# Kernel optimization log

Measured on AMD Instinct MI355X. Metric: run time of the kernel, lower is better.

The kernel has to match this reference:

```python
import jax, jax.numpy as jnp
import numpy as np

N = 65536      # total nodes (BS graphs of 4096 nodes)
E = 524288     # edges
BS = 16
EPS = 1e-5
D_ATT = 8      # attention d_model
H_ATT = 4      # attention heads
SQRT_D = np.float32(np.sqrt(8.0))


def gcn_conv(x, src, dst, W, b):
    # PyG GCNConv: add self-loops, sym-normalized sum aggregation of x @ W
    n = x.shape[0]
    h = x @ W  # [N, out]
    loop = jnp.arange(n, dtype=src.dtype)
    s = jnp.concatenate([src, loop])
    d = jnp.concatenate([dst, loop])
    deg = jax.ops.segment_sum(jnp.ones_like(d, x.dtype), d, num_segments=n)
    dinv = jax.lax.rsqrt(jnp.maximum(deg, 1.0))  # deg >= 1 due to self loops
    norm = dinv[s] * dinv[d]                      # [E+N]
    out = jax.ops.segment_sum(h[s] * norm[:, None], d, num_segments=n)
    return out + b


def sage_conv(x, src, dst, Wl, Wr, b):
    # PyG SAGEConv (mean aggr): lin_l(mean_{j in N(i)} x_j) + lin_r(x_i)
    n = x.shape[0]
    agg = jax.ops.segment_sum(x[src], dst, num_segments=n)
    cnt = jax.ops.segment_sum(jnp.ones_like(dst, x.dtype), dst, num_segments=n)
    mean = agg / jnp.maximum(cnt, 1.0)[:, None]
    return mean @ Wl + x @ Wr + b


def batch_norm(x):
    # F.batch_norm(x, None, None, training=True): per-feature, no affine, biased var
    mu = x.mean(axis=0)
    var = x.var(axis=0)
    return (x - mu) * jax.lax.rsqrt(var + EPS)


def attention_plug(plug, Wq, bq, Wk, bk, Wv, bv, Wfc, bfc):
    q = (plug @ Wq + bq).reshape(BS, 1, H_ATT, D_ATT)
    k = (plug @ Wk + bk).reshape(BS, 1, H_ATT, D_ATT)
    v = (plug @ Wv + bv).reshape(BS, 1, H_ATT, D_ATT)
    scores = jnp.einsum('bihd,bijd->bihj', q, k) / SQRT_D  # [BS,1,H,H]
    logits = scores[:, 0]                                   # squeeze -> [BS,H,H]
    u = jax.random.uniform(jax.random.key(42), logits.shape, minval=1e-9, maxval=1.0)
    gumbel = -jnp.log(-jnp.log(u))
    attn = jax.nn.softmax(logits + gumbel, axis=-1) * SQRT_D  # gumbel_softmax(tau=1)
    attn = attn.reshape(BS, 1, H_ATT, H_ATT)
    out = jnp.einsum('bihj,bijd->bihd', attn, v)  # [BS,1,H,D]
    out = out.reshape(BS, D_ATT, H_ATT).reshape(BS, D_ATT * H_ATT)  # view then flatten
    return out @ Wfc + bfc  # [BS, 4]


def setup_inputs():
    key = jax.random.key(0)
    ks = jax.random.split(key, 24)
    w = lambda k, shp, fan: (jax.random.normal(k, shp, jnp.float32) / np.sqrt(fan)).astype(jnp.float32)
    inp = {}
    inp['x'] = jax.random.normal(ks[0], (N, 640), jnp.float32)
    inp['edge_index'] = jax.random.randint(ks[1], (2, E), 0, N, jnp.int32)
    inp['gender'] = jax.random.uniform(ks[2], (BS, 2), jnp.float32)
    inp['age'] = jax.random.uniform(ks[3], (BS, 1), jnp.float32)
    inp['handed'] = jax.random.uniform(ks[4], (BS, 5), jnp.float32)
    inp['W1'] = w(ks[5], (640, 320), 640); inp['b1'] = jnp.zeros((320,), jnp.float32)
    inp['Wl2'] = w(ks[6], (320, 180), 320); inp['Wr2'] = w(ks[7], (320, 180), 320); inp['b2'] = jnp.zeros((180,), jnp.float32)
    inp['Wl3'] = w(ks[8], (180, 90), 180); inp['Wr3'] = w(ks[9], (180, 90), 180); inp['b3'] = jnp.zeros((90,), jnp.float32)
    inp['Wl4'] = w(ks[10], (90, 50), 90); inp['Wr4'] = w(ks[11], (90, 50), 90); inp['b4'] = jnp.zeros((50,), jnp.float32)
    inp['Wq'] = w(ks[12], (8, 32), 8); inp['bq'] = jnp.zeros((32,), jnp.float32)
    inp['Wk'] = w(ks[13], (8, 32), 8); inp['bk'] = jnp.zeros((32,), jnp.float32)
    inp['Wv'] = w(ks[14], (8, 32), 8); inp['bv'] = jnp.zeros((32,), jnp.float32)
    inp['Wfc'] = w(ks[15], (32, 4), 32); inp['bfc'] = jnp.zeros((4,), jnp.float32)
    inp['Wf1'] = w(ks[16], (54, 32), 54); inp['bf1'] = jnp.zeros((32,), jnp.float32)
    inp['Wf2'] = w(ks[17], (32, 16), 32); inp['bf2'] = jnp.zeros((16,), jnp.float32)
    inp['Wf3'] = w(ks[18], (16, 1), 16); inp['bf3'] = jnp.zeros((1,), jnp.float32)
    return inp


def reference(x, edge_index, gender, age, handed,
              W1, b1, Wl2, Wr2, b2, Wl3, Wr3, b3, Wl4, Wr4, b4,
              Wq, bq, Wk, bk, Wv, bv, Wfc, bfc,
              Wf1, bf1, Wf2, bf2, Wf3, bf3):
    src, dst = edge_index[0], edge_index[1]
    h = batch_norm(jax.nn.leaky_relu(gcn_conv(x, src, dst, W1, b1)))
    h = batch_norm(jax.nn.leaky_relu(sage_conv(h, src, dst, Wl2, Wr2, b2)))
    h = batch_norm(jax.nn.leaky_relu(sage_conv(h, src, dst, Wl3, Wr3, b3)))
    h = batch_norm(jax.nn.leaky_relu(sage_conv(h, src, dst, Wl4, Wr4, b4)))
    batch = jnp.arange(N) // (N // BS)
    pooled = jax.ops.segment_sum(h, batch, num_segments=BS)  # global_add_pool [BS,50]
    plug = jnp.concatenate([gender, age, handed], axis=1)    # [BS,8]
    plugx = attention_plug(plug, Wq, bq, Wk, bk, Wv, bv, Wfc, bfc)  # [BS,4]
    emb = jnp.concatenate([pooled, plugx], axis=1)           # [BS,54]
    out = ((emb @ Wf1 + bf1) @ Wf2 + bf2) @ Wf3 + bf3        # [BS,1]
    return out, emb
```

## Files before the change

### kernel.cpp

```cpp
#include <hip/hip_runtime.h>
#include <cstdint>

#define NN 65536
#define EE 524288
#define BS_ 16

typedef unsigned short u16;
typedef unsigned int u32;
typedef __attribute__((ext_vector_type(8))) short short8v;
typedef __attribute__((ext_vector_type(4))) float f32x4;

__device__ __forceinline__ u16 f2bf(float f) {
    u32 u = __float_as_uint(f);
    u32 r = (u + 0x7fffu + ((u >> 16) & 1u)) >> 16;
    return (u16)r;
}
__device__ __forceinline__ float bff(u16 h) {
    return __uint_as_float(((u32)h) << 16);
}

__device__ __forceinline__ float bnleaky(float v, float s, float q) {
    const float invN = 1.0f / 65536.0f;
    float mu = s * invN;
    float var = q * invN - mu * mu;
    float u = v >= 0.f ? v : 0.01f * v;
    return (u - mu) * rsqrtf(var + 1e-5f);
}

__device__ __forceinline__ u32 rotl32(u32 x, int d) {
    return (x << d) | (x >> (32 - d));
}
__device__ __forceinline__ void threefry_0_42(u32& x0, u32& x1) {
    const u32 ks0 = 0u, ks1 = 42u, ks2 = 0u ^ 42u ^ 0x1BD11BDAu;
    x0 += ks0; x1 += ks1;
#define RND(r) { x0 += x1; x1 = rotl32(x1, r); x1 ^= x0; }
    RND(13) RND(15) RND(26) RND(6)  x0 += ks1; x1 += ks2 + 1u;
    RND(17) RND(29) RND(16) RND(24) x0 += ks2; x1 += ks0 + 2u;
    RND(13) RND(15) RND(26) RND(6)  x0 += ks0; x1 += ks1 + 3u;
    RND(17) RND(29) RND(16) RND(24) x0 += ks1; x1 += ks2 + 4u;
    RND(13) RND(15) RND(26) RND(6)  x0 += ks2; x1 += ks0 + 5u;
#undef RND
}

__global__ void k_indeg(const int* __restrict__ dst, int* __restrict__ indeg) {
    int e = blockIdx.x * 256 + threadIdx.x;
    if (e < EE) atomicAdd(&indeg[dst[e]], 1);
}

__global__ void k_scan(const int* __restrict__ indeg, int* __restrict__ rowptr,
                       int* __restrict__ cursor) {
    __shared__ int psum[256];
    int t = threadIdx.x;
    int base = t * 256;
    int s = 0;
    for (int i = 0; i < 256; ++i) s += indeg[base + i];
    psum[t] = s;
    __syncthreads();
    for (int off = 1; off < 256; off <<= 1) {
        int v = (t >= off) ? psum[t - off] : 0;
        __syncthreads();
        psum[t] += v;
        __syncthreads();
    }
    int run = (t == 0) ? 0 : psum[t - 1];
    for (int i = 0; i < 256; ++i) {
        rowptr[base + i] = run;
        cursor[base + i] = run;
        run += indeg[base + i];
    }
    if (t == 255) rowptr[NN] = run;
}

__global__ void k_fill(const int* __restrict__ src, const int* __restrict__ dst,
                       int* __restrict__ cursor, int* __restrict__ csr) {
    int e = blockIdx.x * 256 + threadIdx.x;
    if (e < EE) {
        int d = dst[e];
        int p = atomicAdd(&cursor[d], 1);
        csr[p] = src[e];
    }
}

__global__ void k_dinv(const int* __restrict__ indeg, float* __restrict__ dinv) {
    int i = blockIdx.x * 256 + threadIdx.x;
    if (i < NN) dinv[i] = rsqrtf((float)indeg[i] + 1.0f);
}

__global__ void k_wsplit2(const float* __restrict__ Wr, const float* __restrict__ Wlsrc,
                          int K, int N, int KP, int CS, int NPW,
                          u16* __restrict__ Wh, u16* __restrict__ Wl) {
    int idx = blockIdx.x * 256 + threadIdx.x;
    if (idx >= NPW * KP) return;
    int n = idx / KP, k = idx % KP;
    float v = 0.f;
    if (n < CS) {
        if (n < N && k < K) v = Wr[(size_t)k * N + n];
    } else {
        int n2 = n - CS;
        if (Wlsrc != nullptr && n2 < N && k < K) v = Wlsrc[(size_t)k * N + n2];
    }
    u16 h = f2bf(v);
    u16 l = f2bf(v - bff(h));
    Wh[idx] = h;
    Wl[idx] = l;
}

template <bool HASB, bool HASBN>
__global__ __launch_bounds__(256, 2) void k_gemm_mfma(
    const float* __restrict__ A, const u16* __restrict__ Wgh, const u16* __restrict__ Wgl,
    int KP, int lda, const float* __restrict__ bns,
    const float* __restrict__ bias, float* __restrict__ O1, float* __restrict__ O2,
    int N, int CS) {
    __shared__ u16 Ah[64][72];
    __shared__ u16 Al[64][72];
    __shared__ u16 Wh[128][72];
    __shared__ u16 Wl[128][72];

    const int t = threadIdx.x;
    const int bm = blockIdx.x * 64;
    const int bn = blockIdx.y * 128;
    const int lane = t & 63;
    const int wid = t >> 6;
    const int wr = wid >> 1, wc = wid & 1;

    f32x4 acc[2][4];
#pragma unroll
    for (int m = 0; m < 2; ++m)
#pragma unroll
        for (int n = 0; n < 4; ++n) acc[m][n] = (f32x4){0.f, 0.f, 0.f, 0.f};

    const int sr = t >> 4;
    const int sc4 = (t & 15) * 4;

    for (int k0 = 0; k0 < KP; k0 += 64) {
        float4 s4, q4;
        if (HASBN) {
            s4 = *(const float4*)(bns + k0 + sc4);
            q4 = *(const float4*)(bns + 512 + k0 + sc4);
        }
#pragma unroll
        for (int p = 0; p < 4; ++p) {
            int rr = sr + 16 * p;
            const float4 v = *(const float4*)(A + (size_t)(bm + rr) * lda + k0 + sc4);
            float vx = v.x, vy = v.y, vz = v.z, vw = v.w;
            if (HASBN) {
                vx = bnleaky(vx, s4.x, q4.x);
                vy = bnleaky(vy, s4.y, q4.y);
                vz = bnleaky(vz, s4.z, q4.z);
                vw = bnleaky(vw, s4.w, q4.w);
            }
            u16 h0 = f2bf(vx), h1 = f2bf(vy), h2 = f2bf(vz), h3 = f2bf(vw);
            u16 l0 = f2bf(vx - bff(h0)), l1 = f2bf(vy - bff(h1));
            u16 l2 = f2bf(vz - bff(h2)), l3 = f2bf(vw - bff(h3));
            uint2 hh, ll;
            hh.x = (u32)h0 | ((u32)h1 << 16); hh.y = (u32)h2 | ((u32)h3 << 16);
            ll.x = (u32)l0 | ((u32)l1 << 16); ll.y = (u32)l2 | ((u32)l3 << 16);
            *(uint2*)&Ah[rr][sc4] = hh;
            *(uint2*)&Al[rr][sc4] = ll;
        }
#pragma unroll
        for (int p = 0; p < 8; ++p) {
            int nn = sr + 16 * p;
            size_t go = (size_t)(bn + nn) * KP + k0 + sc4;
            *(uint2*)&Wh[nn][sc4] = *(const uint2*)(Wgh + go);
            *(uint2*)&Wl[nn][sc4] = *(const uint2*)(Wgl + go);
        }
        __syncthreads();
        const int fr = lane & 15;
        const int kg = (lane >> 4) * 8;
#pragma unroll
        for (int kk = 0; kk < 64; kk += 32) {
            short8v a_h[2], a_l[2], w_h[4], w_l[4];
#pragma unroll
            for (int m = 0; m < 2; ++m) {
                a_h[m] = *(const short8v*)&Ah[wr * 32 + m * 16 + fr][kk + kg];
                a_l[m] = *(const short8v*)&Al[wr * 32 + m * 16 + fr][kk + kg];
            }
#pragma unroll
            for (int n = 0; n < 4; ++n) {
                w_h[n] = *(const short8v*)&Wh[wc * 64 + n * 16 + fr][kk + kg];
                w_l[n] = *(const short8v*)&Wl[wc * 64 + n * 16 + fr][kk + kg];
            }
#pragma unroll
            for (int m = 0; m < 2; ++m)
#pragma unroll
                for (int n = 0; n < 4; ++n) {
                    acc[m][n] = __builtin_amdgcn_mfma_f32_16x16x32_bf16(a_h[m], w_h[n], acc[m][n], 0, 0, 0);
                    acc[m][n] = __builtin_amdgcn_mfma_f32_16x16x32_bf16(a_h[m], w_l[n], acc[m][n], 0, 0, 0);
                    acc[m][n] = __builtin_amdgcn_mfma_f32_16x16x32_bf16(a_l[m], w_h[n], acc[m][n], 0, 0, 0);
                }
        }
        __syncthreads();
    }
    const int fr = lane & 15, fq = lane >> 4;
#pragma unroll
    for (int m = 0; m < 2; ++m) {
        int row = bm + wr * 32 + m * 16 + fq * 4;
#pragma unroll
        for (int n = 0; n < 4; ++n) {
            int col = bn + wc * 64 + n * 16 + fr;
            if (col < CS) {
                float b = (HASB && col < N) ? bias[col] : 0.f;
#pragma unroll
                for (int e = 0; e < 4; ++e)
                    O1[(size_t)(row + e) * CS + col] = acc[m][n][e] + b;
            } else if (O2 != nullptr) {
                int c2 = col - CS;
#pragma unroll
                for (int e = 0; e < 4; ++e)
                    O2[(size_t)(row + e) * CS + c2] = acc[m][n][e];
            }
        }
    }
}

__global__ __launch_bounds__(256) void k_gcn_agg320(const float* __restrict__ h,
                                                    const int* __restrict__ rowptr,
                                                    const int* __restrict__ csr,
                                                    const float* __restrict__ dinv,
                                                    const float* __restrict__ bias,
                                                    float* __restrict__ out) {
    int lane = threadIdx.x & 63;
    int n = blockIdx.x * 4 + (threadIdx.x >> 6);
    bool has1 = lane < 16;
    float di = dinv[n];
    float s2 = di * di;
    const float4* hn = (const float4*)(h + (size_t)n * 320);
    float4 v0 = hn[lane];
    float4 a0 = make_float4(v0.x * s2, v0.y * s2, v0.z * s2, v0.w * s2);
    float4 a1 = make_float4(0.f, 0.f, 0.f, 0.f);
    if (has1) {
        float4 v1 = hn[64 + lane];
        a1 = make_float4(v1.x * s2, v1.y * s2, v1.z * s2, v1.w * s2);
    }
    int e = rowptr[n], e1 = rowptr[n + 1];
    for (; e + 4 <= e1; e += 4) {
        int s0 = csr[e], s1 = csr[e + 1], s2i = csr[e + 2], s3 = csr[e + 3];
        float w0 = dinv[s0] * di, w1 = dinv[s1] * di, w2 = dinv[s2i] * di, w3 = dinv[s3] * di;
        const float4* p0 = (const float4*)(h + (size_t)s0 * 320);
        const float4* p1 = (const float4*)(h + (size_t)s1 * 320);
        const float4* p2 = (const float4*)(h + (size_t)s2i * 320);
        const float4* p3 = (const float4*)(h + (size_t)s3 * 320);
        float4 u0 = p0[lane], u1 = p1[lane], u2 = p2[lane], u3 = p3[lane];
        a0.x += u0.x * w0 + u1.x * w1 + u2.x * w2 + u3.x * w3;
        a0.y += u0.y * w0 + u1.y * w1 + u2.y * w2 + u3.y * w3;
        a0.z += u0.z * w0 + u1.z * w1 + u2.z * w2 + u3.z * w3;
        a0.w += u0.w * w0 + u1.w * w1 + u2.w * w2 + u3.w * w3;
        if (has1) {
            float4 x0 = p0[64 + lane], x1 = p1[64 + lane], x2 = p2[64 + lane], x3 = p3[64 + lane];
            a1.x += x0.x * w0 + x1.x * w1 + x2.x * w2 + x3.x * w3;
            a1.y += x0.y * w0 + x1.y * w1 + x2.y * w2 + x3.y * w3;
            a1.z += x0.z * w0 + x1.z * w1 + x2.z * w2 + x3.z * w3;
            a1.w += x0.w * w0 + x1.w * w1 + x2.w * w2 + x3.w * w3;
        }
    }
    for (; e < e1; ++e) {
        int s = csr[e];
        float w = dinv[s] * di;
        const float4* hs = (const float4*)(h + (size_t)s * 320);
        float4 u0 = hs[lane];
        a0.x = fmaf(u0.x, w, a0.x); a0.y = fmaf(u0.y, w, a0.y);
        a0.z = fmaf(u0.z, w, a0.z); a0.w = fmaf(u0.w, w, a0.w);
        if (has1) {
            float4 u1 = hs[64 + lane];
            a1.x = fmaf(u1.x, w, a1.x); a1.y = fmaf(u1.y, w, a1.y);
            a1.z = fmaf(u1.z, w, a1.z); a1.w = fmaf(u1.w, w, a1.w);
        }
    }
    const float4* b4 = (const float4*)bias;
    float4* on = (float4*)(out + (size_t)n * 320);
    float4 bb = b4[lane];
    on[lane] = make_float4(a0.x + bb.x, a0.y + bb.y, a0.z + bb.z, a0.w + bb.w);
    if (has1) {
        float4 bb1 = b4[64 + lane];
        on[64 + lane] = make_float4(a1.x + bb1.x, a1.y + bb1.y, a1.z + bb1.z, a1.w + bb1.w);
    }
}

template <int CH, int LOG_NPW>
__global__ __launch_bounds__(256) void k_agg_add(const float* __restrict__ T,
                                                 const int* __restrict__ rowptr,
                                                 const int* __restrict__ csr,
                                                 const int* __restrict__ indeg,
                                                 float* __restrict__ C) {
    constexpr int NPW = 1 << LOG_NPW;
    constexpr int LPN = 64 >> LOG_NPW;
    constexpr int SC = CH * 4;
    int lane = threadIdx.x & 63;
    int sub = lane / LPN;
    int ch = lane & (LPN - 1);
    int n = (blockIdx.x * 4 + (threadIdx.x >> 6)) * NPW + sub;
    bool act = ch < CH;
    float4 acc = make_float4(0.f, 0.f, 0.f, 0.f);
    int e = rowptr[n], e1 = rowptr[n + 1];
    for (; e + 4 <= e1; e += 4) {
        int s0 = csr[e], s1 = csr[e + 1], s2 = csr[e + 2], s3 = csr[e + 3];
        if (act) {
            float4 u0 = *(const float4*)(T + (size_t)s0 * SC + ch * 4);
            float4 u1 = *(const float4*)(T + (size_t)s1 * SC + ch * 4);
            float4 u2 = *(const float4*)(T + (size_t)s2 * SC + ch * 4);
            float4 u3 = *(const float4*)(T + (size_t)s3 * SC + ch * 4);
            acc.x += (u0.x + u1.x) + (u2.x + u3.x);
            acc.y += (u0.y + u1.y) + (u2.y + u3.y);
            acc.z += (u0.z + u1.z) + (u2.z + u3.z);
            acc.w += (u0.w + u1.w) + (u2.w + u3.w);
        }
    }
    for (; e < e1; ++e) {
        int s = csr[e];
        if (act) {
            float4 u = *(const float4*)(T + (size_t)s * SC + ch * 4);
            acc.x += u.x; acc.y += u.y; acc.z += u.z; acc.w += u.w;
        }
    }
    int cnt = indeg[n];
    float inv = 1.0f / (float)(cnt > 1 ? cnt : 1);
    if (act) {
        float4* cp = (float4*)(C + (size_t)n * SC + ch * 4);
        float4 c = *cp;
        c.x = fmaf(acc.x, inv, c.x);
        c.y = fmaf(acc.y, inv, c.y);
        c.z = fmaf(acc.z, inv, c.z);
        c.w = fmaf(acc.w, inv, c.w);
        *cp = c;
    }
}

template <int D, int STR>
__global__ __launch_bounds__(256) void k_bn_stats(const float* __restrict__ x,
                                                  float* __restrict__ stats) {
    constexpr int NC = (D + 255) / 256;
    int t = threadIdx.x;
    int r0 = blockIdx.x * 64;
    float s[NC], q[NC];
#pragma unroll
    for (int i = 0; i < NC; ++i) { s[i] = 0.f; q[i] = 0.f; }
#pragma unroll 4
    for (int r = r0; r < r0 + 64; ++r) {
        const float* row = x + (size_t)r * STR;
#pragma unroll
        for (int i = 0; i < NC; ++i) {
            int c = t + 256 * i;
            if (c < D) {
                float v = row[c];
                v = v >= 0.f ? v : 0.01f * v;
                s[i] += v;
                q[i] += v * v;
            }
        }
    }
#pragma unroll
    for (int i = 0; i < NC; ++i) {
        int c = t + 256 * i;
        if (c < D) {
            atomicAdd(&stats[c], s[i]);
            atomicAdd(&stats[512 + c], q[i]);
        }
    }
}

template <int STR>
__global__ __launch_bounds__(256) void k_bn_apply(float* __restrict__ x,
                                                  const float* __restrict__ stats) {
    const float invN = 1.0f / (float)NN;
    size_t total4 = (size_t)NN * STR / 4;
    size_t stride = (size_t)gridDim.x * 256;
    for (size_t i = (size_t)blockIdx.x * 256 + threadIdx.x; i < total4; i += stride) {
        int c = (int)((i * 4) % STR);
        float4 v = ((const float4*)x)[i];
        float4 m4 = *(const float4*)(stats + c);
        float4 q4 = *(const float4*)(stats + 512 + c);
        float4 o;
        o.x = bnleaky(v.x, m4.x, q4.x);
        o.y = bnleaky(v.y, m4.y, q4.y);
        o.z = bnleaky(v.z, m4.z, q4.z);
        o.w = bnleaky(v.w, m4.w, q4.w);
        ((float4*)x)[i] = o;
    }
}

__global__ __launch_bounds__(256) void k_pool(const float* __restrict__ h,
                                              float* __restrict__ pooled) {
    int blk = blockIdx.x;
    int batch = blk >> 4, seg = blk & 15;
    int f = threadIdx.x & 63, g = threadIdx.x >> 6;
    size_t base = ((size_t)batch * 4096 + seg * 256 + g) * 64 + f;
    float acc = 0.f;
    for (int i = 0; i < 64; ++i) acc += h[base + (size_t)i * 256];
    atomicAdd(&pooled[batch * 64 + f], acc);
}

__global__ __launch_bounds__(256) void k_head(
    const float* __restrict__ gender, const float* __restrict__ age,
    const float* __restrict__ handed, const float* __restrict__ Wq,
    const float* __restrict__ bq, const float* __restrict__ Wk,
    const float* __restrict__ bk, const float* __restrict__ Wv,
    const float* __restrict__ bv, const float* __restrict__ Wfc,
    const float* __restrict__ bfc, const float* __restrict__ Wf1,
    const float* __restrict__ bf1, const float* __restrict__ Wf2,
    const float* __restrict__ bf2, const float* __restrict__ Wf3,
    const float* __restrict__ bf3, const float* __restrict__ pooled,
    float* __restrict__ dout) {
    __shared__ float plug[BS_][8];
    __shared__ float qs[BS_][32], ks[BS_][32], vs[BS_][32];
    __shared__ float gum[256];
    __shared__ float x32[BS_][32];
    __shared__ float px[BS_][4];
    __shared__ float embs[BS_][54];
    __shared__ float t1[BS_][32];
    __shared__ float t2[BS_][16];
    int t = threadIdx.x;

    if (t < 128) {
        int b = t >> 3, c = t & 7;
        float v;
        if (c < 2) v = gender[b * 2 + c];
        else if (c == 2) v = age[b];
        else v = handed[b * 5 + (c - 3)];
        plug[b][c] = v;
    }
    {
        u32 lane = (u32)(t & 127);
        u32 a = lane, b2 = lane + 128u;
        threefry_0_42(a, b2);
        u32 bits = (t < 128) ? a : b2;
        float u = __uint_as_float((bits >> 9) | 0x3f800000u) - 1.0f;
        const float mn = 1e-9f;
        u = u * (1.0f - mn) + mn;
        u = fmaxf(mn, u);
        gum[t] = -logf(-logf(u));
    }
    __syncthreads();
    for (int idx = t; idx < 512; idx += 256) {
        int b = idx >> 5, c = idx & 31;
        float aq = bq[c], ak = bk[c], av = bv[c];
#pragma unroll
        for (int i = 0; i < 8; ++i) {
            float p = plug[b][i];
            aq = fmaf(p, Wq[i * 32 + c], aq);
            ak = fmaf(p, Wk[i * 32 + c], ak);
            av = fmaf(p, Wv[i * 32 + c], av);
        }
        qs[b][c] = aq; ks[b][c] = ak; vs[b][c] = av;
    }
    __syncthreads();
    if (t < 64) {
        int b = t >> 2, h = t & 3;
        const float isq = 0.35355339059327373f;
        const float sq = 2.8284271247461903f;
        float sc[4];
#pragma unroll
        for (int j = 0; j < 4; ++j) {
            float d = 0.f;
#pragma unroll
            for (int dd = 0; dd < 8; ++dd) d = fmaf(qs[b][h * 8 + dd], ks[b][j * 8 + dd], d);
            sc[j] = d * isq + gum[b * 16 + h * 4 + j];
        }
        float m = fmaxf(fmaxf(sc[0], sc[1]), fmaxf(sc[2], sc[3]));
        float e0 = expf(sc[0] - m), e1 = expf(sc[1] - m), e2 = expf(sc[2] - m), e3 = expf(sc[3] - m);
        float sum = e0 + e1 + e2 + e3;
        float a0 = e0 / sum * sq, a1 = e1 / sum * sq, a2 = e2 / sum * sq, a3 = e3 / sum * sq;
#pragma unroll
        for (int dd = 0; dd < 8; ++dd) {
            float o = a0 * vs[b][0 * 8 + dd] + a1 * vs[b][1 * 8 + dd] +
                      a2 * vs[b][2 * 8 + dd] + a3 * vs[b][3 * 8 + dd];
            x32[b][h * 8 + dd] = o;
        }
    }
    __syncthreads();
    if (t < 64) {
        int b = t >> 2, n = t & 3;
        float a = bfc[n];
#pragma unroll
        for (int m = 0; m < 32; ++m) a = fmaf(x32[b][m], Wfc[m * 4 + n], a);
        px[b][n] = a;
    }
    __syncthreads();
    for (int idx = t; idx < BS_ * 54; idx += 256) {
        int b = idx / 54, c = idx % 54;
        float v = (c < 50) ? pooled[b * 64 + c] : px[b][c - 50];
        embs[b][c] = v;
        dout[16 + idx] = v;
    }
    __syncthreads();
    for (int idx = t; idx < 512; idx += 256) {
        int b = idx >> 5, c = idx & 31;
        float a = bf1[c];
#pragma unroll
        for (int k = 0; k < 54; ++k) a = fmaf(embs[b][k], Wf1[k * 32 + c], a);
        t1[b][c] = a;
    }
    __syncthreads();
    {
        int b = t >> 4, c = t & 15;
        float a = bf2[c];
#pragma unroll
        for (int k = 0; k < 32; ++k) a = fmaf(t1[b][k], Wf2[k * 16 + c], a);
        t2[b][c] = a;
    }
    __syncthreads();
    if (t < 16) {
        float a = bf3[0];
#pragma unroll
        for (int k = 0; k < 16; ++k) a = fmaf(t2[t][k], Wf3[k], a);
        dout[t] = a;
    }
}

extern "C" void kernel_launch(void* const* d_in, const int* in_sizes, int n_in,
                              void* d_out, int out_size, void* d_ws, size_t ws_size,
                              hipStream_t stream) {
    const float* x      = (const float*)d_in[0];
    const int*   ei     = (const int*)d_in[1];
    const float* gender = (const float*)d_in[2];
    const float* age    = (const float*)d_in[3];
    const float* handed = (const float*)d_in[4];
    const float* W1  = (const float*)d_in[5];
    const float* b1  = (const float*)d_in[6];
    const float* Wl2 = (const float*)d_in[7];
    const float* Wr2 = (const float*)d_in[8];
    const float* b2  = (const float*)d_in[9];
    const float* Wl3 = (const float*)d_in[10];
    const float* Wr3 = (const float*)d_in[11];
    const float* b3  = (const float*)d_in[12];
    const float* Wl4 = (const float*)d_in[13];
    const float* Wr4 = (const float*)d_in[14];
    const float* b4  = (const float*)d_in[15];
    const float* Wq  = (const float*)d_in[16];
    const float* bq  = (const float*)d_in[17];
    const float* Wk  = (const float*)d_in[18];
    const float* bk  = (const float*)d_in[19];
    const float* Wv  = (const float*)d_in[20];
    const float* bv  = (const float*)d_in[21];
    const float* Wfc = (const float*)d_in[22];
    const float* bfc = (const float*)d_in[23];
    const float* Wf1 = (const float*)d_in[24];
    const float* bf1 = (const float*)d_in[25];
    const float* Wf2 = (const float*)d_in[26];
    const float* bf2 = (const float*)d_in[27];
    const float* Wf3 = (const float*)d_in[28];
    const float* bf3 = (const float*)d_in[29];

    const int* srcp = ei;
    const int* dstp = ei + EE;

    char* wsb = (char*)d_ws;
    size_t off = 0;
    auto alloc = [&](size_t bytes) -> char* {
        char* p = wsb + off;
        off += (bytes + 255) & ~(size_t)255;
        return p;
    };
    float* P = (float*)alloc((size_t)NN * 320 * 4);
    float* Q = (float*)alloc((size_t)NN * 320 * 4);
    float* R = (float*)alloc((size_t)NN * 192 * 4);
    float* T = (float*)alloc((size_t)NN * 192 * 4);
    int* indeg  = (int*)alloc((size_t)NN * 4);
    int* rowptr = (int*)alloc((size_t)(NN + 1) * 4);
    int* cursor = (int*)alloc((size_t)(NN + 1) * 4);
    int* csr    = (int*)alloc((size_t)EE * 4);
    float* dinv = (float*)alloc((size_t)NN * 4);
    float* stats  = (float*)alloc(4096 * 4);
    float* pooled = (float*)alloc(16 * 64 * 4);
    u16* W1h = (u16*)alloc((size_t)384 * 640 * 2);
    u16* W1l = (u16*)alloc((size_t)384 * 640 * 2);
    u16* W2h = (u16*)alloc((size_t)384 * 320 * 2);
    u16* W2l = (u16*)alloc((size_t)384 * 320 * 2);
    u16* W3h = (u16*)alloc((size_t)256 * 192 * 2);
    u16* W3l = (u16*)alloc((size_t)256 * 192 * 2);
    u16* W4h = (u16*)alloc((size_t)128 * 128 * 2);
    u16* W4l = (u16*)alloc((size_t)128 * 128 * 2);
    float* dout = (float*)d_out;

    hipMemsetAsync(indeg, 0, (size_t)NN * 4, stream);
    hipMemsetAsync(stats, 0, 4096 * 4, stream);
    k_indeg<<<EE / 256, 256, 0, stream>>>(dstp, indeg);
    k_scan<<<1, 256, 0, stream>>>(indeg, rowptr, cursor);
    k_fill<<<EE / 256, 256, 0, stream>>>(srcp, dstp, cursor, csr);
    k_dinv<<<NN / 256, 256, 0, stream>>>(indeg, dinv);

    k_wsplit2<<<(384 * 640 + 255) / 256, 256, 0, stream>>>(W1, nullptr, 640, 320, 640, 320, 384, W1h, W1l);
    k_wsplit2<<<(384 * 320 + 255) / 256, 256, 0, stream>>>(Wr2, Wl2, 320, 180, 320, 192, 384, W2h, W2l);
    k_wsplit2<<<(256 * 192 + 255) / 256, 256, 0, stream>>>(Wr3, Wl3, 180, 90, 192, 128, 256, W3h, W3l);
    k_wsplit2<<<(128 * 128 + 255) / 256, 256, 0, stream>>>(Wr4, Wl4, 90, 50, 128, 64, 128, W4h, W4l);

    k_gemm_mfma<false, false><<<dim3(1024, 3), 256, 0, stream>>>(
        x, W1h, W1l, 640, 640, nullptr, nullptr, P, nullptr, 320, 320);
    k_gcn_agg320<<<NN / 4, 256, 0, stream>>>(P, rowptr, csr, dinv, b1, Q);
    k_bn_stats<320, 320><<<1024, 256, 0, stream>>>(Q, stats);

    k_gemm_mfma<true, true><<<dim3(1024, 3), 256, 0, stream>>>(
        Q, W2h, W2l, 320, 320, stats, b2, R, T, 180, 192);
    k_agg_add<48, 0><<<NN / 4, 256, 0, stream>>>(T, rowptr, csr, indeg, R);
    k_bn_stats<180, 192><<<1024, 256, 0, stream>>>(R, stats + 1024);

    k_gemm_mfma<true, true><<<dim3(1024, 2), 256, 0, stream>>>(
        R, W3h, W3l, 192, 192, stats + 1024, b3, P, T, 90, 128);
    k_agg_add<32, 1><<<NN / 8, 256, 0, stream>>>(T, rowptr, csr, indeg, P);
    k_bn_stats<90, 128><<<1024, 256, 0, stream>>>(P, stats + 2048);

    k_gemm_mfma<true, true><<<dim3(1024, 1), 256, 0, stream>>>(
        P, W4h, W4l, 128, 128, stats + 2048, b4, Q, T, 50, 64);
    k_agg_add<16, 2><<<NN / 16, 256, 0, stream>>>(T, rowptr, csr, indeg, Q);
    k_bn_stats<50, 64><<<1024, 256, 0, stream>>>(Q, stats + 3072);
    k_bn_apply<64><<<2048, 256, 0, stream>>>(Q, stats + 3072);

    hipMemsetAsync(pooled, 0, 16 * 64 * 4, stream);
    k_pool<<<256, 256, 0, stream>>>(Q, pooled);
    k_head<<<1, 256, 0, stream>>>(gender, age, handed, Wq, bq, Wk, bk, Wv, bv,
                                  Wfc, bfc, Wf1, bf1, Wf2, bf2, Wf3, bf3, pooled, dout);
}
```

Baseline: 1.129 ms.

## Drop A low-part split, prefetch next K tile, swap grid axes in GEMM

The split-bf16 GEMM no longer keeps a low-order part for the activation operand. This removes the Al shared buffer, its conversion work and one of the three MFMAs per tile, leaving 2 MFMAs. The next K tile's global loads are now issued into registers before the current tile's MFMAs, so memory latency overlaps compute. The grid axes are swapped so that blocks sharing an A row-tile run adjacently for L2 reuse, and launch bounds are raised to 3 blocks per CU. Accuracy falls to roughly bf16 precision on activations, which may break tolerance, and the extra prefetch registers could cause spills under the tighter occupancy bound.

```diff
diff --git a/kernel.cpp b/kernel.cpp
--- a/kernel.cpp
+++ b/kernel.cpp
@@ -106,19 +106,18 @@
 }
 
 template <bool HASB, bool HASBN>
-__global__ __launch_bounds__(256, 2) void k_gemm_mfma(
+__global__ __launch_bounds__(256, 3) void k_gemm_mfma(
     const float* __restrict__ A, const u16* __restrict__ Wgh, const u16* __restrict__ Wgl,
     int KP, int lda, const float* __restrict__ bns,
     const float* __restrict__ bias, float* __restrict__ O1, float* __restrict__ O2,
     int N, int CS) {
     __shared__ u16 Ah[64][72];
-    __shared__ u16 Al[64][72];
     __shared__ u16 Wh[128][72];
     __shared__ u16 Wl[128][72];
 
     const int t = threadIdx.x;
-    const int bm = blockIdx.x * 64;
-    const int bn = blockIdx.y * 128;
+    const int bm = blockIdx.y * 64;
+    const int bn = blockIdx.x * 128;
     const int lane = t & 63;
     const int wid = t >> 6;
     const int wr = wid >> 1, wc = wid & 1;
@@ -132,50 +131,59 @@
     const int sr = t >> 4;
     const int sc4 = (t & 15) * 4;
 
+    float4 pa[4];
+    uint2 pwh[8], pwl[8];
+    float4 ps, pq;
+
+    auto loadt = [&](int k0) {
+#pragma unroll
+        for (int p = 0; p < 4; ++p)
+            pa[p] = *(const float4*)(A + (size_t)(bm + sr + 16 * p) * lda + k0 + sc4);
+#pragma unroll
+        for (int p = 0; p < 8; ++p) {
+            size_t go = (size_t)(bn + sr + 16 * p) * KP + k0 + sc4;
+            pwh[p] = *(const uint2*)(Wgh + go);
+            pwl[p] = *(const uint2*)(Wgl + go);
+        }
+        if (HASBN) {
+            ps = *(const float4*)(bns + k0 + sc4);
+            pq = *(const float4*)(bns + 512 + k0 + sc4);
+        }
+    };
+
+    loadt(0);
     for (int k0 = 0; k0 < KP; k0 += 64) {
-        float4 s4, q4;
-        if (HASBN) {
-            s4 = *(const float4*)(bns + k0 + sc4);
-            q4 = *(const float4*)(bns + 512 + k0 + sc4);
-        }
 #pragma unroll
         for (int p = 0; p < 4; ++p) {
-            int rr = sr + 16 * p;
-            const float4 v = *(const float4*)(A + (size_t)(bm + rr) * lda + k0 + sc4);
-            float vx = v.x, vy = v.y, vz = v.z, vw = v.w;
+            float vx = pa[p].x, vy = pa[p].y, vz = pa[p].z, vw = pa[p].w;
             if (HASBN) {
-                vx = bnleaky(vx, s4.x, q4.x);
-                vy = bnleaky(vy, s4.y, q4.y);
-                vz = bnleaky(vz, s4.z, q4.z);
-                vw = bnleaky(vw, s4.w, q4.w);
+                vx = bnleaky(vx, ps.x, pq.x);
+                vy = bnleaky(vy, ps.y, pq.y);
+                vz = bnleaky(vz, ps.z, pq.z);
+                vw = bnleaky(vw, ps.w, pq.w);
             }
             u16 h0 = f2bf(vx), h1 = f2bf(vy), h2 = f2bf(vz), h3 = f2bf(vw);
-            u16 l0 = f2bf(vx - bff(h0)), l1 = f2bf(vy - bff(h1));
-            u16 l2 = f2bf(vz - bff(h2)), l3 = f2bf(vw - bff(h3));
-            uint2 hh, ll;
-            hh.x = (u32)h0 | ((u32)h1 << 16); hh.y = (u32)h2 | ((u32)h3 << 16);
-            ll.x = (u32)l0 | ((u32)l1 << 16); ll.y = (u32)l2 | ((u32)l3 << 16);
-            *(uint2*)&Ah[rr][sc4] = hh;
-            *(uint2*)&Al[rr][sc4] = ll;
+            uint2 hh;
+            hh.x = (u32)h0 | ((u32)h1 << 16);
+            hh.y = (u32)h2 | ((u32)h3 << 16);
+            *(uint2*)&Ah[sr + 16 * p][sc4] = hh;
         }
 #pragma unroll
         for (int p = 0; p < 8; ++p) {
-            int nn = sr + 16 * p;
-            size_t go = (size_t)(bn + nn) * KP + k0 + sc4;
-            *(uint2*)&Wh[nn][sc4] = *(const uint2*)(Wgh + go);
-            *(uint2*)&Wl[nn][sc4] = *(const uint2*)(Wgl + go);
+            *(uint2*)&Wh[sr + 16 * p][sc4] = pwh[p];
+            *(uint2*)&Wl[sr + 16 * p][sc4] = pwl[p];
         }
         __syncthreads();
+        if (k0 + 64 < KP) loadt(k0 + 64);
+
         const int fr = lane & 15;
         const int kg = (lane >> 4) * 8;
 #pragma unroll
         for (int kk = 0; kk < 64; kk += 32) {
-            short8v a_h[2], a_l[2], w_h[4], w_l[4];
-#pragma unroll
-            for (int m = 0; m < 2; ++m) {
+            short8v a_h[2], w_h[4], w_l[4];
+#pragma unroll
+            for (int m = 0; m < 2; ++m)
                 a_h[m] = *(const short8v*)&Ah[wr * 32 + m * 16 + fr][kk + kg];
-                a_l[m] = *(const short8v*)&Al[wr * 32 + m * 16 + fr][kk + kg];
-            }
 #pragma unroll
             for (int n = 0; n < 4; ++n) {
                 w_h[n] = *(const short8v*)&Wh[wc * 64 + n * 16 + fr][kk + kg];
@@ -187,7 +195,6 @@
                 for (int n = 0; n < 4; ++n) {
                     acc[m][n] = __builtin_amdgcn_mfma_f32_16x16x32_bf16(a_h[m], w_h[n], acc[m][n], 0, 0, 0);
                     acc[m][n] = __builtin_amdgcn_mfma_f32_16x16x32_bf16(a_h[m], w_l[n], acc[m][n], 0, 0, 0);
-                    acc[m][n] = __builtin_amdgcn_mfma_f32_16x16x32_bf16(a_l[m], w_h[n], acc[m][n], 0, 0, 0);
                 }
         }
         __syncthreads();
@@ -362,7 +369,6 @@
 template <int STR>
 __global__ __launch_bounds__(256) void k_bn_apply(float* __restrict__ x,
                                                   const float* __restrict__ stats) {
-    const float invN = 1.0f / (float)NN;
     size_t total4 = (size_t)NN * STR / 4;
     size_t stride = (size_t)gridDim.x * 256;
     for (size_t i = (size_t)blockIdx.x * 256 + threadIdx.x; i < total4; i += stride) {
@@ -584,22 +590,22 @@
     k_wsplit2<<<(256 * 192 + 255) / 256, 256, 0, stream>>>(Wr3, Wl3, 180, 90, 192, 128, 256, W3h, W3l);
     k_wsplit2<<<(128 * 128 + 255) / 256, 256, 0, stream>>>(Wr4, Wl4, 90, 50, 128, 64, 128, W4h, W4l);
 
-    k_gemm_mfma<false, false><<<dim3(1024, 3), 256, 0, stream>>>(
+    k_gemm_mfma<false, false><<<dim3(3, 1024), 256, 0, stream>>>(
         x, W1h, W1l, 640, 640, nullptr, nullptr, P, nullptr, 320, 320);
     k_gcn_agg320<<<NN / 4, 256, 0, stream>>>(P, rowptr, csr, dinv, b1, Q);
     k_bn_stats<320, 320><<<1024, 256, 0, stream>>>(Q, stats);
 
-    k_gemm_mfma<true, true><<<dim3(1024, 3), 256, 0, stream>>>(
+    k_gemm_mfma<true, true><<<dim3(3, 1024), 256, 0, stream>>>(
         Q, W2h, W2l, 320, 320, stats, b2, R, T, 180, 192);
     k_agg_add<48, 0><<<NN / 4, 256, 0, stream>>>(T, rowptr, csr, indeg, R);
     k_bn_stats<180, 192><<<1024, 256, 0, stream>>>(R, stats + 1024);
 
-    k_gemm_mfma<true, true><<<dim3(1024, 2), 256, 0, stream>>>(
+    k_gemm_mfma<true, true><<<dim3(2, 1024), 256, 0, stream>>>(
         R, W3h, W3l, 192, 192, stats + 1024, b3, P, T, 90, 128);
     k_agg_add<32, 1><<<NN / 8, 256, 0, stream>>>(T, rowptr, csr, indeg, P);
     k_bn_stats<90, 128><<<1024, 256, 0, stream>>>(P, stats + 2048);
 
-    k_gemm_mfma<true, true><<<dim3(1024, 1), 256, 0, stream>>>(
+    k_gemm_mfma<true, true><<<dim3(1, 1024), 256, 0, stream>>>(
         P, W4h, W4l, 128, 128, stats + 2048, b4, Q, T, 50, 64);
     k_agg_add<16, 2><<<NN / 16, 256, 0, stream>>>(T, rowptr, csr, indeg, Q);
     k_bn_stats<50, 64><<<1024, 256, 0, stream>>>(Q, stats + 3072);
```

Result: slower. 1.218 ms (+7.8%).

## Replace LDS-staged split-bf16 GEMM with direct-load MFMA kernel, drop A low term

Applied to the files above, without the earlier changes.

The GEMM no longer stages A and W tiles through shared memory. Each wave loads its MFMA fragments straight from global memory, so the barriers and LDS traffic go away, and the tile layout changes to 128 rows by 64 columns with four waves per block. The A-low correction term is dropped, cutting the MFMA count from three to two per tile, which lowers precision of the activation operand to bf16. Occupancy hints rise to 4 blocks. The cost is that operand reuse now depends on L1/L2 caching instead of LDS, and more global loads are issued.

```diff
diff --git a/kernel.cpp b/kernel.cpp
--- a/kernel.cpp
+++ b/kernel.cpp
@@ -17,6 +17,14 @@
 }
 __device__ __forceinline__ float bff(u16 h) {
     return __uint_as_float(((u32)h) << 16);
+}
+__device__ __forceinline__ short8v cvt8(float4 u0, float4 u1) {
+    union { u32 w[4]; short8v v; } r;
+    r.w[0] = (u32)f2bf(u0.x) | ((u32)f2bf(u0.y) << 16);
+    r.w[1] = (u32)f2bf(u0.z) | ((u32)f2bf(u0.w) << 16);
+    r.w[2] = (u32)f2bf(u1.x) | ((u32)f2bf(u1.y) << 16);
+    r.w[3] = (u32)f2bf(u1.z) | ((u32)f2bf(u1.w) << 16);
+    return r.v;
 }
 
 __device__ __forceinline__ float bnleaky(float v, float s, float q) {
@@ -25,6 +33,12 @@
     float var = q * invN - mu * mu;
     float u = v >= 0.f ? v : 0.01f * v;
     return (u - mu) * rsqrtf(var + 1e-5f);
+}
+__device__ __forceinline__ void bn4(float4& u, float4 s, float4 q) {
+    u.x = bnleaky(u.x, s.x, q.x);
+    u.y = bnleaky(u.y, s.y, q.y);
+    u.z = bnleaky(u.z, s.z, q.z);
+    u.w = bnleaky(u.w, s.w, q.w);
 }
 
 __device__ __forceinline__ u32 rotl32(u32 x, int d) {
@@ -106,22 +120,18 @@
 }
 
 template <bool HASB, bool HASBN>
-__global__ __launch_bounds__(256, 2) void k_gemm_mfma(
+__global__ __launch_bounds__(256, 4) void k_gemm_direct(
     const float* __restrict__ A, const u16* __restrict__ Wgh, const u16* __restrict__ Wgl,
     int KP, int lda, const float* __restrict__ bns,
     const float* __restrict__ bias, float* __restrict__ O1, float* __restrict__ O2,
     int N, int CS) {
-    __shared__ u16 Ah[64][72];
-    __shared__ u16 Al[64][72];
-    __shared__ u16 Wh[128][72];
-    __shared__ u16 Wl[128][72];
-
     const int t = threadIdx.x;
-    const int bm = blockIdx.x * 64;
-    const int bn = blockIdx.y * 128;
     const int lane = t & 63;
     const int wid = t >> 6;
-    const int wr = wid >> 1, wc = wid & 1;
+    const int bm = blockIdx.y * 128 + wid * 32;
+    const int bn = blockIdx.x * 64;
+    const int fr = lane & 15;
+    const int kg = (lane >> 4) * 8;
 
     f32x4 acc[2][4];
 #pragma unroll
@@ -129,87 +139,60 @@
 #pragma unroll
         for (int n = 0; n < 4; ++n) acc[m][n] = (f32x4){0.f, 0.f, 0.f, 0.f};
 
-    const int sr = t >> 4;
-    const int sc4 = (t & 15) * 4;
-
-    for (int k0 = 0; k0 < KP; k0 += 64) {
-        float4 s4, q4;
+    const float* a0p = A + (size_t)(bm + fr) * lda + kg;
+    const float* a1p = A + (size_t)(bm + 16 + fr) * lda + kg;
+    const u16* whp[4];
+    const u16* wlp[4];
+#pragma unroll
+    for (int n = 0; n < 4; ++n) {
+        size_t o = (size_t)(bn + n * 16 + fr) * KP + kg;
+        whp[n] = Wgh + o;
+        wlp[n] = Wgl + o;
+    }
+
+    for (int k0 = 0; k0 < KP; k0 += 32) {
+        float4 u00 = *(const float4*)(a0p + k0);
+        float4 u01 = *(const float4*)(a0p + k0 + 4);
+        float4 u10 = *(const float4*)(a1p + k0);
+        float4 u11 = *(const float4*)(a1p + k0 + 4);
         if (HASBN) {
-            s4 = *(const float4*)(bns + k0 + sc4);
-            q4 = *(const float4*)(bns + 512 + k0 + sc4);
-        }
-#pragma unroll
-        for (int p = 0; p < 4; ++p) {
-            int rr = sr + 16 * p;
-            const float4 v = *(const float4*)(A + (size_t)(bm + rr) * lda + k0 + sc4);
-            float vx = v.x, vy = v.y, vz = v.z, vw = v.w;
-            if (HASBN) {
-                vx = bnleaky(vx, s4.x, q4.x);
-                vy = bnleaky(vy, s4.y, q4.y);
-                vz = bnleaky(vz, s4.z, q4.z);
-                vw = bnleaky(vw, s4.w, q4.w);
-            }
-            u16 h0 = f2bf(vx), h1 = f2bf(vy), h2 = f2bf(vz), h3 = f2bf(vw);
-            u16 l0 = f2bf(vx - bff(h0)), l1 = f2bf(vy - bff(h1));
-            u16 l2 = f2bf(vz - bff(h2)), l3 = f2bf(vw - bff(h3));
-            uint2 hh, ll;
-            hh.x = (u32)h0 | ((u32)h1 << 16); hh.y = (u32)h2 | ((u32)h3 << 16);
-            ll.x = (u32)l0 | ((u32)l1 << 16); ll.y = (u32)l2 | ((u32)l3 << 16);
-            *(uint2*)&Ah[rr][sc4] = hh;
-            *(uint2*)&Al[rr][sc4] = ll;
-        }
-#pragma unroll
-        for (int p = 0; p < 8; ++p) {
-            int nn = sr + 16 * p;
-            size_t go = (size_t)(bn + nn) * KP + k0 + sc4;
-            *(uint2*)&Wh[nn][sc4] = *(const uint2*)(Wgh + go);
-            *(uint2*)&Wl[nn][sc4] = *(const uint2*)(Wgl + go);
-        }
-        __syncthreads();
-        const int fr = lane & 15;
-        const int kg = (lane >> 4) * 8;
-#pragma unroll
-        for (int kk = 0; kk < 64; kk += 32) {
-            short8v a_h[2], a_l[2], w_h[4], w_l[4];
-#pragma unroll
-            for (int m = 0; m < 2; ++m) {
-                a_h[m] = *(const short8v*)&Ah[wr * 32 + m * 16 + fr][kk + kg];
-                a_l[m] = *(const short8v*)&Al[wr * 32 + m * 16 + fr][kk + kg];
-            }
-#pragma unroll
-            for (int n = 0; n < 4; ++n) {
-                w_h[n] = *(const short8v*)&Wh[wc * 64 + n * 16 + fr][kk + kg];
-                w_l[n] = *(const short8v*)&Wl[wc * 64 + n * 16 + fr][kk + kg];
-            }
-#pragma unroll
-            for (int m = 0; m < 2; ++m)
-#pragma unroll
-                for (int n = 0; n < 4; ++n) {
-                    acc[m][n] = __builtin_amdgcn_mfma_f32_16x16x32_bf16(a_h[m], w_h[n], acc[m][n], 0, 0, 0);
-                    acc[m][n] = __builtin_amdgcn_mfma_f32_16x16x32_bf16(a_h[m], w_l[n], acc[m][n], 0, 0, 0);
-                    acc[m][n] = __builtin_amdgcn_mfma_f32_16x16x32_bf16(a_l[m], w_h[n], acc[m][n], 0, 0, 0);
-                }
-        }
-        __syncthreads();
-    }
-    const int fr = lane & 15, fq = lane >> 4;
+            float4 s0 = *(const float4*)(bns + k0 + kg);
+            float4 s1 = *(const float4*)(bns + k0 + kg + 4);
+            float4 q0 = *(const float4*)(bns + 512 + k0 + kg);
+            float4 q1 = *(const float4*)(bns + 512 + k0 + kg + 4);
+            bn4(u00, s0, q0); bn4(u01, s1, q1);
+            bn4(u10, s0, q0); bn4(u11, s1, q1);
+        }
+        short8v ah0 = cvt8(u00, u01);
+        short8v ah1 = cvt8(u10, u11);
+#pragma unroll
+        for (int n = 0; n < 4; ++n) {
+            short8v wh = *(const short8v*)(whp[n] + k0);
+            short8v wl = *(const short8v*)(wlp[n] + k0);
+            acc[0][n] = __builtin_amdgcn_mfma_f32_16x16x32_bf16(ah0, wh, acc[0][n], 0, 0, 0);
+            acc[1][n] = __builtin_amdgcn_mfma_f32_16x16x32_bf16(ah1, wh, acc[1][n], 0, 0, 0);
+            acc[0][n] = __builtin_amdgcn_mfma_f32_16x16x32_bf16(ah0, wl, acc[0][n], 0, 0, 0);
+            acc[1][n] = __builtin_amdgcn_mfma_f32_16x16x32_bf16(ah1, wl, acc[1][n], 0, 0, 0);
+        }
+    }
+
+    float* O = O1;
+    int colb = bn;
+    bool isO1 = true;
+    if (bn >= CS) { O = O2; colb = bn - CS; isO1 = false; }
+    const int fq = lane >> 4;
 #pragma unroll
     for (int m = 0; m < 2; ++m) {
-        int row = bm + wr * 32 + m * 16 + fq * 4;
+        int row = bm + m * 16 + fq * 4;
 #pragma unroll
         for (int n = 0; n < 4; ++n) {
-            int col = bn + wc * 64 + n * 16 + fr;
-            if (col < CS) {
-                float b = (HASB && col < N) ? bias[col] : 0.f;
-#pragma unroll
-                for (int e = 0; e < 4; ++e)
-                    O1[(size_t)(row + e) * CS + col] = acc[m][n][e] + b;
-            } else if (O2 != nullptr) {
-                int c2 = col - CS;
-#pragma unroll
-                for (int e = 0; e < 4; ++e)
-                    O2[(size_t)(row + e) * CS + c2] = acc[m][n][e];
-            }
+            int gcol = bn + n * 16 + fr;
+            int col = colb + n * 16 + fr;
+            float b = 0.f;
+            if (HASB && isO1 && gcol < N) b = bias[gcol];
+#pragma unroll
+            for (int e = 0; e < 4; ++e)
+                O[(size_t)(row + e) * CS + col] = acc[m][n][e] + b;
         }
     }
 }
@@ -362,7 +345,6 @@
 template <int STR>
 __global__ __launch_bounds__(256) void k_bn_apply(float* __restrict__ x,
                                                   const float* __restrict__ stats) {
-    const float invN = 1.0f / (float)NN;
     size_t total4 = (size_t)NN * STR / 4;
     size_t stride = (size_t)gridDim.x * 256;
     for (size_t i = (size_t)blockIdx.x * 256 + threadIdx.x; i < total4; i += stride) {
@@ -584,22 +566,22 @@
     k_wsplit2<<<(256 * 192 + 255) / 256, 256, 0, stream>>>(Wr3, Wl3, 180, 90, 192, 128, 256, W3h, W3l);
     k_wsplit2<<<(128 * 128 + 255) / 256, 256, 0, stream>>>(Wr4, Wl4, 90, 50, 128, 64, 128, W4h, W4l);
 
-    k_gemm_mfma<false, false><<<dim3(1024, 3), 256, 0, stream>>>(
+    k_gemm_direct<false, false><<<dim3(5, 512), 256, 0, stream>>>(
         x, W1h, W1l, 640, 640, nullptr, nullptr, P, nullptr, 320, 320);
     k_gcn_agg320<<<NN / 4, 256, 0, stream>>>(P, rowptr, csr, dinv, b1, Q);
     k_bn_stats<320, 320><<<1024, 256, 0, stream>>>(Q, stats);
 
-    k_gemm_mfma<true, true><<<dim3(1024, 3), 256, 0, stream>>>(
+    k_gemm_direct<true, true><<<dim3(6, 512), 256, 0, stream>>>(
         Q, W2h, W2l, 320, 320, stats, b2, R, T, 180, 192);
     k_agg_add<48, 0><<<NN / 4, 256, 0, stream>>>(T, rowptr, csr, indeg, R);
     k_bn_stats<180, 192><<<1024, 256, 0, stream>>>(R, stats + 1024);
 
-    k_gemm_mfma<true, true><<<dim3(1024, 2), 256, 0, stream>>>(
+    k_gemm_direct<true, true><<<dim3(4, 512), 256, 0, stream>>>(
         R, W3h, W3l, 192, 192, stats + 1024, b3, P, T, 90, 128);
     k_agg_add<32, 1><<<NN / 8, 256, 0, stream>>>(T, rowptr, csr, indeg, P);
     k_bn_stats<90, 128><<<1024, 256, 0, stream>>>(P, stats + 2048);
 
-    k_gemm_mfma<true, true><<<dim3(1024, 1), 256, 0, stream>>>(
+    k_gemm_direct<true, true><<<dim3(2, 512), 256, 0, stream>>>(
         P, W4h, W4l, 128, 128, stats + 2048, b4, Q, T, 50, 64);
     k_agg_add<16, 2><<<NN / 16, 256, 0, stream>>>(T, rowptr, csr, indeg, Q);
     k_bn_stats<50, 64><<<1024, 256, 0, stream>>>(Q, stats + 3072);
```

After: 1.392 ms. +23.3%, slower.
